# Kernel optimization log

Measured on AMD Instinct MI355X. Metric: run time of the kernel, lower is better.

The kernel has to match this reference:

```python
import jax, jax.numpy as jnp
import numpy as np

B, N, C = 8, 1024, 768
HEADS = 8
HD = C // HEADS  # head_dim = qk_dim // num_heads since qk_ratio=1
SCALE = HD ** (-0.5)


def setup_inputs() -> dict:
    key = jax.random.key(0)
    ks = jax.random.split(key, 8)
    s = 0.02
    return {
        "x": jax.random.normal(ks[0], (B, N, C), dtype=jnp.float32),
        "y": jax.random.normal(ks[1], (B, N, C), dtype=jnp.float32),
        "relative_pos": jax.random.normal(ks[2], (HEADS, N, N), dtype=jnp.float32),
        "H": 32,
        "W": 32,
        "Wq": jax.random.normal(ks[3], (C, C), dtype=jnp.float32) * s,
        "Wk": jax.random.normal(ks[4], (C, C), dtype=jnp.float32) * s,
        "Wv": jax.random.normal(ks[5], (C, C), dtype=jnp.float32) * s,
        "Wp": jax.random.normal(ks[6], (C, C), dtype=jnp.float32) * s,
        "bp": jnp.zeros((C,), dtype=jnp.float32),
    }


def reference(x, y, relative_pos, H, W, Wq, Wk, Wv, Wp, bp):
    # sr_ratio == 1 path: K/V come directly from y (no spatial reduction).
    b, n, c = x.shape
    q = (x @ Wq.T).reshape(b, n, HEADS, HD)       # bnhd
    k = (y @ Wk.T).reshape(b, n, HEADS, HD)       # bmhd
    v = (y @ Wv.T).reshape(b, n, HEADS, HD)       # bmhd
    # scores: QK^T * scale + learned relative position bias (broadcast over batch)
    attn = jnp.einsum("bnhd,bmhd->bhnm", q, k) * SCALE + relative_pos[None]
    attn = jax.nn.softmax(attn, axis=-1)
    out = jnp.einsum("bhnm,bmhd->bnhd", attn, v).reshape(b, n, c)
    return out @ Wp.T + bp
```

## Files before the change

kernel.cpp:

```cpp
#include <hip/hip_runtime.h>
#include <hip/hip_bf16.h>
#include <cstdint>
#include <cstddef>


using f32x4  = __attribute__((ext_vector_type(4))) float;
using bf16x8 = __attribute__((ext_vector_type(8))) __bf16;

constexpr int Bb = 8, Nn = 1024, Cc = 768;
constexpr float LOG2E = 1.4426950408889634f;
constexpr float QSC   = 0.10206207261596575f * 1.4426950408889634f;

__device__ __forceinline__ uint16_t f2bf(float f) {
  union { float f; uint32_t u; } v; v.f = f;
  return (uint16_t)((v.u + 0x7fffu + ((v.u >> 16) & 1u)) >> 16);
}

__device__ __forceinline__ void gl_lds16(const void* g, void* l) {
  __builtin_amdgcn_global_load_lds(
      (const __attribute__((address_space(1))) void*)g,
      (__attribute__((address_space(3))) void*)l, 16, 0, 0);
}

__device__ __forceinline__ f32x4 mfma16(bf16x8 a, bf16x8 b, f32x4 c) {
  return __builtin_amdgcn_mfma_f32_16x16x32_bf16(a, b, c, 0, 0, 0);
}

template <int CTRL>
__device__ __forceinline__ float dpp_add(float v) {
  union { float f; int i; } u, r;
  u.f = v;
  r.i = __builtin_amdgcn_update_dpp(u.i, u.i, CTRL, 0xF, 0xF, false);
  return v + r.f;
}
__device__ __forceinline__ float red16_add(float v) {
  v = dpp_add<0x128>(v);
  v = dpp_add<0x124>(v);
  v = dpp_add<0x122>(v);
  v = dpp_add<0x121>(v);
  return v;
}

__global__ void cvt2_kernel(const float* __restrict__ a,
                            const float* __restrict__ b,
                            uint16_t* __restrict__ da,
                            uint16_t* __restrict__ db, int n4) {
  int i = blockIdx.x * blockDim.x + threadIdx.x;
  const float* s = blockIdx.y ? b : a;
  uint16_t* d = blockIdx.y ? db : da;
  if (i < n4) {
    float4 v = ((const float4*)s)[i];
    ushort4 o;
    o.x = f2bf(v.x); o.y = f2bf(v.y); o.z = f2bf(v.z); o.w = f2bf(v.w);
    ((ushort4*)d)[i] = o;
  }
}

__global__ void cvtw_kernel(const float* __restrict__ wq,
                            const float* __restrict__ wk,
                            const float* __restrict__ wv,
                            const float* __restrict__ wp,
                            uint16_t* __restrict__ dq, uint16_t* __restrict__ dk,
                            uint16_t* __restrict__ dv, uint16_t* __restrict__ dp,
                            int n4) {
  int i = blockIdx.x * blockDim.x + threadIdx.x;
  const float* s; uint16_t* d; float sc = 1.f;
  switch (blockIdx.y) {
    case 0:  s = wq; d = dq; sc = QSC; break;
    case 1:  s = wk; d = dk; break;
    case 2:  s = wv; d = dv; break;
    default: s = wp; d = dp; break;
  }
  if (i < n4) {
    float4 v = ((const float4*)s)[i];
    ushort4 o;
    o.x = f2bf(v.x * sc); o.y = f2bf(v.y * sc);
    o.z = f2bf(v.z * sc); o.w = f2bf(v.w * sc);
    ((ushort4*)d)[i] = o;
  }
}

__device__ __forceinline__ void gemm_core(const uint16_t* __restrict__ A,
                                          const uint16_t* __restrict__ Bt,
                                          int m0, int n0, f32x4 (&acc)[4][4]) {
  __shared__ uint16_t As[2][128 * 64];
  __shared__ uint16_t Bs[2][128 * 64];
  const int tid = threadIdx.x;
  const int lane = tid & 63, l16 = lane & 15, quad = lane >> 4;
  const int w = tid >> 6;
  const int wm = (w & 1) * 64, wn = (w >> 1) * 64;

  int soff[4];
#pragma unroll
  for (int i = 0; i < 4; ++i) {
    int idx = tid + 256 * i;
    int row = idx >> 3, pc = idx & 7;
    int c = pc ^ (row & 7);
    soff[i] = row * 768 + c * 8;
  }

  const uint16_t* Abase = A + (size_t)m0 * 768;
  const uint16_t* Bbase = Bt + (size_t)n0 * 768;
  auto stage = [&](int k0, int buf) {
#pragma unroll
    for (int i = 0; i < 4; ++i)
      gl_lds16(Abase + k0 + soff[i], &As[buf][(tid + 256 * i) * 8]);
#pragma unroll
    for (int i = 0; i < 4; ++i)
      gl_lds16(Bbase + k0 + soff[i], &Bs[buf][(tid + 256 * i) * 8]);
  };

  stage(0, 0);

#pragma unroll 2
  for (int kt = 0; kt < 12; ++kt) {
    const int cur = kt & 1, nxt = (kt + 1) & 1;
    __syncthreads();
    if (kt < 11) stage((kt + 1) * 64, nxt);

#pragma unroll
    for (int ks = 0; ks < 2; ++ks) {
      bf16x8 a[4], b[4];
      const int phys = (ks * 4 + quad) ^ (l16 & 7);
#pragma unroll
      for (int i = 0; i < 4; ++i)
        a[i] = *(const bf16x8*)&As[cur][(wm + i * 16 + l16) * 64 + phys * 8];
#pragma unroll
      for (int j = 0; j < 4; ++j)
        b[j] = *(const bf16x8*)&Bs[cur][(wn + j * 16 + l16) * 64 + phys * 8];
#pragma unroll
      for (int i = 0; i < 4; ++i)
#pragma unroll
        for (int j = 0; j < 4; ++j)
          acc[i][j] = mfma16(a[i], b[j], acc[i][j]);
    }
  }
}

__global__ __launch_bounds__(256, 2) void qkv_kernel(
    const uint16_t* __restrict__ xb, const uint16_t* __restrict__ yb,
    const uint16_t* __restrict__ wq, const uint16_t* __restrict__ wk,
    const uint16_t* __restrict__ wv, uint16_t* __restrict__ Qb,
    uint16_t* __restrict__ Kb, uint16_t* __restrict__ Vt) {
  const int seg = blockIdx.x / 6, nb = blockIdx.x % 6;
  const uint16_t* A  = (seg == 0) ? xb : yb;
  const uint16_t* Bt = (seg == 0) ? wq : (seg == 1) ? wk : wv;
  const int m0 = blockIdx.y * 128, n0 = nb * 128;

  f32x4 acc[4][4] = {};
  gemm_core(A, Bt, m0, n0, acc);

  const int tid = threadIdx.x, lane = tid & 63;
  const int l16 = lane & 15, quad = lane >> 4, w = tid >> 6;
  const int wm = (w & 1) * 64, wn = (w >> 1) * 64;

  if (seg <= 1) {
    uint16_t* O = seg ? Kb : Qb;
#pragma unroll
    for (int i = 0; i < 4; ++i)
#pragma unroll
      for (int j = 0; j < 4; ++j) {
        int col = n0 + wn + j * 16 + l16;
#pragma unroll
        for (int r = 0; r < 4; ++r) {
          int row = m0 + wm + i * 16 + quad * 4 + r;
          O[(size_t)row * 768 + col] = f2bf(acc[i][j][r]);
        }
      }
  } else {
#pragma unroll
    for (int i = 0; i < 4; ++i) {
      int row0 = m0 + wm + i * 16 + quad * 4;
      int bidx = row0 >> 10, nseq = row0 & 1023;
#pragma unroll
      for (int j = 0; j < 4; ++j) {
        int col = n0 + wn + j * 16 + l16;
        int h = col / 96, hd = col % 96;
        ushort4 pk;
        pk.x = f2bf(acc[i][j][0]); pk.y = f2bf(acc[i][j][1]);
        pk.z = f2bf(acc[i][j][2]); pk.w = f2bf(acc[i][j][3]);
        size_t o = (((size_t)(bidx * 8 + h) * 96 + hd) << 10) + nseq;
        *(ushort4*)(Vt + o) = pk;
      }
    }
  }
}

__global__ __launch_bounds__(256, 2) void proj_kernel(
    const uint16_t* __restrict__ A, const uint16_t* __restrict__ Bt,
    float* __restrict__ out, const float* __restrict__ bias) {
  const int m0 = blockIdx.y * 128, n0 = blockIdx.x * 128;
  f32x4 acc[4][4] = {};
  gemm_core(A, Bt, m0, n0, acc);

  const int tid = threadIdx.x, lane = tid & 63;
  const int l16 = lane & 15, quad = lane >> 4, w = tid >> 6;
  const int wm = (w & 1) * 64, wn = (w >> 1) * 64;
  float bv[4];
#pragma unroll
  for (int j = 0; j < 4; ++j) bv[j] = bias[n0 + wn + j * 16 + l16];
#pragma unroll
  for (int i = 0; i < 4; ++i)
#pragma unroll
    for (int j = 0; j < 4; ++j) {
      int col = n0 + wn + j * 16 + l16;
#pragma unroll
      for (int r = 0; r < 4; ++r) {
        int row = m0 + wm + i * 16 + quad * 4 + r;
        out[(size_t)row * 768 + col] = acc[i][j][r] + bv[j];
      }
    }
}

__global__ __launch_bounds__(256, 2) void attn_kernel(
    const uint16_t* __restrict__ Q,
    const uint16_t* __restrict__ Kb,
    const uint16_t* __restrict__ Vt,
    const float* __restrict__ rel,
    uint16_t* __restrict__ AO) {
  __shared__ uint16_t Ks[2][64 * 96];
  __shared__ uint16_t Vs[2][96 * 64];
  __shared__ uint16_t Ps[128 * 64];

  const int tid = threadIdx.x;
  const int q0 = blockIdx.x * 128;
  const int bh = blockIdx.y;
  const int b = bh >> 3, h = bh & 7;
  const int w = tid >> 6, lane = tid & 63;
  const int l16 = lane & 15, quad = lane >> 4;
  const int l7 = l16 & 7;

  bf16x8 qf[2][3];
#pragma unroll
  for (int st = 0; st < 2; ++st) {
    const int qrow = q0 + st * 64 + w * 16 + l16;
    const uint16_t* qp =
        Q + ((size_t)(b * 1024 + qrow)) * 768 + h * 96 + quad * 8;
#pragma unroll
    for (int j = 0; j < 3; ++j) qf[st][j] = *(const bf16x8*)(qp + j * 32);
  }

  auto kSrc = [](int c) {
    int r = c / 12, pc = c % 12;
    int kc = (pc < 8) ? (pc ^ (r & 7)) : (8 + ((pc & 3) ^ (r & 3)));
    return r * 768 + kc * 8;
  };
  auto vSrc = [](int c) {
    int d = c >> 3, pc = c & 7;
    return d * 1024 + (pc ^ (d & 7)) * 8;
  };
  int koffs[3], voffs[3];
#pragma unroll
  for (int i = 0; i < 3; ++i) {
    koffs[i] = kSrc(tid + 256 * i);
    voffs[i] = vSrc(tid + 256 * i);
  }

  const uint16_t* kslab = Kb + ((size_t)(b * 1024)) * 768 + h * 96;
  const uint16_t* vslab = Vt + ((size_t)(bh * 96) << 10);
  const float* relbase0 =
      rel + ((size_t)h << 20) + ((size_t)(q0 + w * 16 + quad * 4) << 10) + l16;
  const float* relbase1 = relbase0 + (64 << 10);

  auto stage = [&](int knext, int bufi) {
    const uint16_t* kb = kslab + (size_t)knext * 768;
    const uint16_t* vb = vslab + knext;
    uint16_t* Kbuf = &Ks[bufi][0];
    uint16_t* Vbuf = &Vs[bufi][0];
#pragma unroll
    for (int i = 0; i < 3; ++i) {
      gl_lds16(kb + koffs[i], Kbuf + (tid + 256 * i) * 8);
      gl_lds16(vb + voffs[i], Vbuf + (tid + 256 * i) * 8);
    }
  };

  float relv[2][16];
  auto loadrel = [&](int knext) {
#pragma unroll
    for (int r = 0; r < 4; ++r)
#pragma unroll
      for (int nt = 0; nt < 4; ++nt) {
        relv[0][nt * 4 + r] = relbase0[(size_t)r * 1024 + knext + nt * 16];
        relv[1][nt * 4 + r] = relbase1[(size_t)r * 1024 + knext + nt * 16];
      }
  };

  float l_i[2][4] = {};
  f32x4 o_acc[2][6] = {};

  stage(0, 0);
  loadrel(0);

#pragma unroll 2
  for (int kt = 0; kt < 16; ++kt) {
    const int cur = kt & 1, nxt = (kt + 1) & 1;
    __syncthreads();
    if (kt < 15) stage((kt + 1) * 64, nxt);
    const uint16_t* KsC = &Ks[cur][0];
    const uint16_t* VsC = &Vs[cur][0];

    f32x4 s[2][4] = {};
#pragma unroll
    for (int ksi = 0; ksi < 3; ++ksi) {
#pragma unroll
      for (int nt = 0; nt < 4; ++nt) {
        const int row = nt * 16 + l16;
        const int c = ksi * 4 + quad;
        const int phys =
            (ksi < 2) ? (c ^ (row & 7)) : (8 + ((c & 3) ^ (row & 3)));
        bf16x8 kf = *(const bf16x8*)&KsC[row * 96 + phys * 8];
        s[0][nt] = mfma16(qf[0][ksi], kf, s[0][nt]);
        s[1][nt] = mfma16(qf[1][ksi], kf, s[1][nt]);
      }
    }

    const int khi = l16 >> 3;
#pragma unroll
    for (int st = 0; st < 2; ++st) {
      float pv[16];
#pragma unroll
      for (int nt = 0; nt < 4; ++nt)
#pragma unroll
        for (int r = 0; r < 4; ++r)
          pv[nt * 4 + r] = __builtin_amdgcn_exp2f(
              fmaf(relv[st][nt * 4 + r], LOG2E, s[st][nt][r]));
#pragma unroll
      for (int r = 0; r < 4; ++r)
        l_i[st][r] += (pv[r] + pv[4 + r]) + (pv[8 + r] + pv[12 + r]);
#pragma unroll
      for (int r = 0; r < 4; ++r) {
        const int qloc = quad * 4 + r;
        const int rowoff = (st * 64 + w * 16 + qloc) * 64;
        const int sw = qloc & 7;
#pragma unroll
        for (int nt = 0; nt < 4; ++nt) {
          const int kc = 2 * nt + khi;
          Ps[rowoff + (((kc ^ sw) << 3) | l7)] = f2bf(pv[nt * 4 + r]);
        }
      }
    }

    if (kt < 15) loadrel((kt + 1) * 64);

    asm volatile("s_waitcnt lgkmcnt(0)" ::: "memory");

#pragma unroll
    for (int ksi = 0; ksi < 2; ++ksi) {
      const int phys = (ksi * 4 + quad) ^ l7;
      bf16x8 pf0 = *(const bf16x8*)&Ps[(w * 16 + l16) * 64 + phys * 8];
      bf16x8 pf1 = *(const bf16x8*)&Ps[(64 + w * 16 + l16) * 64 + phys * 8];
#pragma unroll
      for (int jt = 0; jt < 6; ++jt) {
        const int d = jt * 16 + l16;
        bf16x8 vf = *(const bf16x8*)&VsC[d * 64 + phys * 8];
        o_acc[0][jt] = mfma16(pf0, vf, o_acc[0][jt]);
        o_acc[1][jt] = mfma16(pf1, vf, o_acc[1][jt]);
      }
    }
  }

#pragma unroll
  for (int st = 0; st < 2; ++st)
#pragma unroll
    for (int r = 0; r < 4; ++r) {
      float inv = 1.f / red16_add(l_i[st][r]);
      int row = q0 + st * 64 + w * 16 + quad * 4 + r;
#pragma unroll
      for (int jt = 0; jt < 6; ++jt) {
        int col = h * 96 + jt * 16 + l16;
        AO[(size_t)(b * 1024 + row) * 768 + col] = f2bf(o_acc[st][jt][r] * inv);
      }
    }
}

extern "C" void kernel_launch(void* const* d_in, const int* in_sizes, int n_in,
                              void* d_out, int out_size, void* d_ws,
                              size_t ws_size, hipStream_t stream) {
  const float* x   = (const float*)d_in[0];
  const float* y   = (const float*)d_in[1];
  const float* rel = (const float*)d_in[2];
  const float* Wq  = (const float*)d_in[5];
  const float* Wk  = (const float*)d_in[6];
  const float* Wv  = (const float*)d_in[7];
  const float* Wp  = (const float*)d_in[8];
  const float* bp  = (const float*)d_in[9];
  float* out = (float*)d_out;

  const size_t nBNC = (size_t)Bb * Nn * Cc;
  const size_t nW = (size_t)Cc * Cc;

  char* ws = (char*)d_ws;
  size_t off = 0;
  auto alloc = [&](size_t bytes) {
    char* p = ws + off;
    off += (bytes + 255) & ~(size_t)255;
    return p;
  };
  uint16_t* xb  = (uint16_t*)alloc(nBNC * 2);
  uint16_t* yb  = (uint16_t*)alloc(nBNC * 2);
  uint16_t* wqb = (uint16_t*)alloc(nW * 2);
  uint16_t* wkb = (uint16_t*)alloc(nW * 2);
  uint16_t* wvb = (uint16_t*)alloc(nW * 2);
  uint16_t* wpb = (uint16_t*)alloc(nW * 2);
  uint16_t* Qb  = (uint16_t*)alloc(nBNC * 2);
  uint16_t* Kb  = (uint16_t*)alloc(nBNC * 2);
  uint16_t* Vtb = (uint16_t*)alloc(nBNC * 2);
  uint16_t* AOb = (uint16_t*)alloc(nBNC * 2);

  cvt2_kernel<<<dim3((int)(nBNC / 4 / 256), 2), 256, 0, stream>>>(
      x, y, xb, yb, (int)(nBNC / 4));
  cvtw_kernel<<<dim3((int)(nW / 4 / 256), 4), 256, 0, stream>>>(
      Wq, Wk, Wv, Wp, wqb, wkb, wvb, wpb, (int)(nW / 4));

  qkv_kernel<<<dim3(18, 64), 256, 0, stream>>>(xb, yb, wqb, wkb, wvb, Qb, Kb,
                                               Vtb);

  attn_kernel<<<dim3(8, 64), 256, 0, stream>>>(Qb, Kb, Vtb, rel, AOb);

  proj_kernel<<<dim3(6, 64), 256, 0, stream>>>(AOb, wpb, out, bp);
}
```

Baseline: 256.8 us.

## Merge conversion kernels, single-buffer GEMM, LDS-transpose V store, smaller proj tiles

Merges the two fp32-to-bf16 conversion kernels into one launch. Replaces the double-buffered GEMM K-loop with a single-buffered load/sync/compute loop, which halves LDS use so qkv can run more blocks per CU, at the cost of no longer overlapping loads with MFMA work. The V-transpose store now goes through shared memory, so each lane writes 16-byte contiguous rows instead of scattered 8-byte stores. The projection GEMM uses 64x128 tiles with twice as many blocks and higher occupancy bounds.

Measured after the change: 238.4 us. -7.2%, faster.

```diff
diff --git a/kernel.cpp b/kernel.cpp
--- a/kernel.cpp
+++ b/kernel.cpp
@@ -41,50 +41,42 @@
   return v;
 }
 
-__global__ void cvt2_kernel(const float* __restrict__ a,
-                            const float* __restrict__ b,
-                            uint16_t* __restrict__ da,
-                            uint16_t* __restrict__ db, int n4) {
+constexpr int NX4 = (Bb * Nn * Cc) / 4;
+constexpr int NW4 = (Cc * Cc) / 4;
+__global__ void cvt_all(const float* __restrict__ x, const float* __restrict__ y,
+                        const float* __restrict__ wq, const float* __restrict__ wk,
+                        const float* __restrict__ wv, const float* __restrict__ wp,
+                        uint16_t* __restrict__ xb, uint16_t* __restrict__ yb,
+                        uint16_t* __restrict__ dq, uint16_t* __restrict__ dk,
+                        uint16_t* __restrict__ dv, uint16_t* __restrict__ dp) {
   int i = blockIdx.x * blockDim.x + threadIdx.x;
-  const float* s = blockIdx.y ? b : a;
-  uint16_t* d = blockIdx.y ? db : da;
-  if (i < n4) {
-    float4 v = ((const float4*)s)[i];
-    ushort4 o;
-    o.x = f2bf(v.x); o.y = f2bf(v.y); o.z = f2bf(v.z); o.w = f2bf(v.w);
-    ((ushort4*)d)[i] = o;
-  }
-}
-
-__global__ void cvtw_kernel(const float* __restrict__ wq,
-                            const float* __restrict__ wk,
-                            const float* __restrict__ wv,
-                            const float* __restrict__ wp,
-                            uint16_t* __restrict__ dq, uint16_t* __restrict__ dk,
-                            uint16_t* __restrict__ dv, uint16_t* __restrict__ dp,
-                            int n4) {
-  int i = blockIdx.x * blockDim.x + threadIdx.x;
-  const float* s; uint16_t* d; float sc = 1.f;
-  switch (blockIdx.y) {
-    case 0:  s = wq; d = dq; sc = QSC; break;
-    case 1:  s = wk; d = dk; break;
-    case 2:  s = wv; d = dv; break;
-    default: s = wp; d = dp; break;
-  }
-  if (i < n4) {
-    float4 v = ((const float4*)s)[i];
-    ushort4 o;
-    o.x = f2bf(v.x * sc); o.y = f2bf(v.y * sc);
-    o.z = f2bf(v.z * sc); o.w = f2bf(v.w * sc);
-    ((ushort4*)d)[i] = o;
-  }
+  const float* s; uint16_t* d; int off; float sc = 1.f;
+  if (i < NX4) {
+    s = x; d = xb; off = i;
+  } else if (i < 2 * NX4) {
+    s = y; d = yb; off = i - NX4;
+  } else {
+    int j = i - 2 * NX4;
+    int wsel = j / NW4;
+    off = j - wsel * NW4;
+    switch (wsel) {
+      case 0:  s = wq; d = dq; sc = QSC; break;
+      case 1:  s = wk; d = dk; break;
+      case 2:  s = wv; d = dv; break;
+      default: s = wp; d = dp; break;
+    }
+  }
+  float4 v = ((const float4*)s)[off];
+  ushort4 o;
+  o.x = f2bf(v.x * sc); o.y = f2bf(v.y * sc);
+  o.z = f2bf(v.z * sc); o.w = f2bf(v.w * sc);
+  ((ushort4*)d)[off] = o;
 }
 
 __device__ __forceinline__ void gemm_core(const uint16_t* __restrict__ A,
                                           const uint16_t* __restrict__ Bt,
+                                          uint16_t* As, uint16_t* Bs,
                                           int m0, int n0, f32x4 (&acc)[4][4]) {
-  __shared__ uint16_t As[2][128 * 64];
-  __shared__ uint16_t Bs[2][128 * 64];
   const int tid = threadIdx.x;
   const int lane = tid & 63, l16 = lane & 15, quad = lane >> 4;
   const int w = tid >> 6;
@@ -99,24 +91,15 @@
     soff[i] = row * 768 + c * 8;
   }
 
-  const uint16_t* Abase = A + (size_t)m0 * 768;
-  const uint16_t* Bbase = Bt + (size_t)n0 * 768;
-  auto stage = [&](int k0, int buf) {
+  for (int k0 = 0; k0 < 768; k0 += 64) {
+    __syncthreads();
 #pragma unroll
     for (int i = 0; i < 4; ++i)
-      gl_lds16(Abase + k0 + soff[i], &As[buf][(tid + 256 * i) * 8]);
+      gl_lds16(A + (size_t)m0 * 768 + k0 + soff[i], &As[(tid + 256 * i) * 8]);
 #pragma unroll
     for (int i = 0; i < 4; ++i)
-      gl_lds16(Bbase + k0 + soff[i], &Bs[buf][(tid + 256 * i) * 8]);
-  };
-
-  stage(0, 0);
-
-#pragma unroll 2
-  for (int kt = 0; kt < 12; ++kt) {
-    const int cur = kt & 1, nxt = (kt + 1) & 1;
-    __syncthreads();
-    if (kt < 11) stage((kt + 1) * 64, nxt);
+      gl_lds16(Bt + (size_t)n0 * 768 + k0 + soff[i], &Bs[(tid + 256 * i) * 8]);
+    __syncthreads();
 
 #pragma unroll
     for (int ks = 0; ks < 2; ++ks) {
@@ -124,10 +107,10 @@
       const int phys = (ks * 4 + quad) ^ (l16 & 7);
 #pragma unroll
       for (int i = 0; i < 4; ++i)
-        a[i] = *(const bf16x8*)&As[cur][(wm + i * 16 + l16) * 64 + phys * 8];
+        a[i] = *(const bf16x8*)&As[(wm + i * 16 + l16) * 64 + phys * 8];
 #pragma unroll
       for (int j = 0; j < 4; ++j)
-        b[j] = *(const bf16x8*)&Bs[cur][(wn + j * 16 + l16) * 64 + phys * 8];
+        b[j] = *(const bf16x8*)&Bs[(wn + j * 16 + l16) * 64 + phys * 8];
 #pragma unroll
       for (int i = 0; i < 4; ++i)
 #pragma unroll
@@ -137,18 +120,19 @@
   }
 }
 
-__global__ __launch_bounds__(256, 2) void qkv_kernel(
+__global__ __launch_bounds__(256, 3) void qkv_kernel(
     const uint16_t* __restrict__ xb, const uint16_t* __restrict__ yb,
     const uint16_t* __restrict__ wq, const uint16_t* __restrict__ wk,
     const uint16_t* __restrict__ wv, uint16_t* __restrict__ Qb,
     uint16_t* __restrict__ Kb, uint16_t* __restrict__ Vt) {
+  __shared__ uint16_t smem[128 * 130];
   const int seg = blockIdx.x / 6, nb = blockIdx.x % 6;
   const uint16_t* A  = (seg == 0) ? xb : yb;
   const uint16_t* Bt = (seg == 0) ? wq : (seg == 1) ? wk : wv;
   const int m0 = blockIdx.y * 128, n0 = nb * 128;
 
   f32x4 acc[4][4] = {};
-  gemm_core(A, Bt, m0, n0, acc);
+  gemm_core(A, Bt, smem, smem + 8192, m0, n0, acc);
 
   const int tid = threadIdx.x, lane = tid & 63;
   const int l16 = lane & 15, quad = lane >> 4, w = tid >> 6;
@@ -168,39 +152,90 @@
         }
       }
   } else {
-#pragma unroll
-    for (int i = 0; i < 4; ++i) {
-      int row0 = m0 + wm + i * 16 + quad * 4;
-      int bidx = row0 >> 10, nseq = row0 & 1023;
+    __syncthreads();
+#pragma unroll
+    for (int i = 0; i < 4; ++i)
 #pragma unroll
       for (int j = 0; j < 4; ++j) {
-        int col = n0 + wn + j * 16 + l16;
-        int h = col / 96, hd = col % 96;
+        int ml = wm + i * 16 + quad * 4;
+        int nl = wn + j * 16 + l16;
         ushort4 pk;
         pk.x = f2bf(acc[i][j][0]); pk.y = f2bf(acc[i][j][1]);
         pk.z = f2bf(acc[i][j][2]); pk.w = f2bf(acc[i][j][3]);
-        size_t o = (((size_t)(bidx * 8 + h) * 96 + hd) << 10) + nseq;
-        *(ushort4*)(Vt + o) = pk;
-      }
-    }
-  }
-}
-
-__global__ __launch_bounds__(256, 2) void proj_kernel(
+        *(ushort4*)&smem[nl * 130 + ml] = pk;
+      }
+    __syncthreads();
+    const int bidx = m0 >> 10, nseq0 = m0 & 1023;
+#pragma unroll
+    for (int pass = 0; pass < 8; ++pass) {
+      int nl = pass * 16 + (tid >> 4);
+      int col = n0 + nl;
+      int h = col / 96, hd = col % 96;
+      int m = (tid & 15) * 8;
+      bf16x8 v = *(const bf16x8*)&smem[nl * 130 + m];
+      size_t o = (((size_t)(bidx * 8 + h) * 96 + hd) << 10) + nseq0 + m;
+      *(bf16x8*)(Vt + o) = v;
+    }
+  }
+}
+
+__global__ __launch_bounds__(256, 4) void proj_kernel(
     const uint16_t* __restrict__ A, const uint16_t* __restrict__ Bt,
     float* __restrict__ out, const float* __restrict__ bias) {
-  const int m0 = blockIdx.y * 128, n0 = blockIdx.x * 128;
-  f32x4 acc[4][4] = {};
-  gemm_core(A, Bt, m0, n0, acc);
-
+  __shared__ uint16_t As[64 * 64];
+  __shared__ uint16_t Bs[128 * 64];
+  const int m0 = blockIdx.y * 64, n0 = blockIdx.x * 128;
   const int tid = threadIdx.x, lane = tid & 63;
   const int l16 = lane & 15, quad = lane >> 4, w = tid >> 6;
-  const int wm = (w & 1) * 64, wn = (w >> 1) * 64;
+  const int wm = (w & 1) * 32, wn = (w >> 1) * 64;
+
+  int soffA[2], soffB[4];
+#pragma unroll
+  for (int i = 0; i < 2; ++i) {
+    int idx = tid + 256 * i;
+    int row = idx >> 3, pc = idx & 7;
+    soffA[i] = row * 768 + (pc ^ (row & 7)) * 8;
+  }
+#pragma unroll
+  for (int i = 0; i < 4; ++i) {
+    int idx = tid + 256 * i;
+    int row = idx >> 3, pc = idx & 7;
+    soffB[i] = row * 768 + (pc ^ (row & 7)) * 8;
+  }
+
+  f32x4 acc[2][4] = {};
+  for (int k0 = 0; k0 < 768; k0 += 64) {
+    __syncthreads();
+#pragma unroll
+    for (int i = 0; i < 2; ++i)
+      gl_lds16(A + (size_t)m0 * 768 + k0 + soffA[i], &As[(tid + 256 * i) * 8]);
+#pragma unroll
+    for (int i = 0; i < 4; ++i)
+      gl_lds16(Bt + (size_t)n0 * 768 + k0 + soffB[i], &Bs[(tid + 256 * i) * 8]);
+    __syncthreads();
+#pragma unroll
+    for (int ks = 0; ks < 2; ++ks) {
+      bf16x8 a[2], b[4];
+      const int phys = (ks * 4 + quad) ^ (l16 & 7);
+#pragma unroll
+      for (int i = 0; i < 2; ++i)
+        a[i] = *(const bf16x8*)&As[(wm + i * 16 + l16) * 64 + phys * 8];
+#pragma unroll
+      for (int j = 0; j < 4; ++j)
+        b[j] = *(const bf16x8*)&Bs[(wn + j * 16 + l16) * 64 + phys * 8];
+#pragma unroll
+      for (int i = 0; i < 2; ++i)
+#pragma unroll
+        for (int j = 0; j < 4; ++j)
+          acc[i][j] = mfma16(a[i], b[j], acc[i][j]);
+    }
+  }
+
   float bv[4];
 #pragma unroll
   for (int j = 0; j < 4; ++j) bv[j] = bias[n0 + wn + j * 16 + l16];
 #pragma unroll
-  for (int i = 0; i < 4; ++i)
+  for (int i = 0; i < 2; ++i)
 #pragma unroll
     for (int j = 0; j < 4; ++j) {
       int col = n0 + wn + j * 16 + l16;
@@ -407,15 +442,14 @@
   uint16_t* Vtb = (uint16_t*)alloc(nBNC * 2);
   uint16_t* AOb = (uint16_t*)alloc(nBNC * 2);
 
-  cvt2_kernel<<<dim3((int)(nBNC / 4 / 256), 2), 256, 0, stream>>>(
-      x, y, xb, yb, (int)(nBNC / 4));
-  cvtw_kernel<<<dim3((int)(nW / 4 / 256), 4), 256, 0, stream>>>(
-      Wq, Wk, Wv, Wp, wqb, wkb, wvb, wpb, (int)(nW / 4));
+  const int cvtBlocks = (2 * NX4 + 4 * NW4) / 256;
+  cvt_all<<<cvtBlocks, 256, 0, stream>>>(x, y, Wq, Wk, Wv, Wp, xb, yb, wqb,
+                                         wkb, wvb, wpb);
 
   qkv_kernel<<<dim3(18, 64), 256, 0, stream>>>(xb, yb, wqb, wkb, wvb, Qb, Kb,
                                                Vtb);
 
   attn_kernel<<<dim3(8, 64), 256, 0, stream>>>(Qb, Kb, Vtb, rel, AOb);
 
-  proj_kernel<<<dim3(6, 64), 256, 0, stream>>>(AOb, wpb, out, bp);
-}
+  proj_kernel<<<dim3(6, 128), 256, 0, stream>>>(AOb, wpb, out, bp);
+}
```
